# Kernel tuning notes

Hardware: AMD Instinct MI355X
Metric: run time of the kernel (lower is better)

## Reference

```python
import jax, jax.numpy as jnp
import numpy as np

B, T, I, H = 32768, 200, 6, 6
FF, OUT = 128, 12


def setup_inputs() -> dict:
    key = jax.random.key(0)
    ks = jax.random.split(key, 10)
    s = lambda fan_in: 1.0 / np.sqrt(fan_in)
    inp = {
        "x": jax.random.normal(ks[0], (B, T, I), dtype=jnp.float32),
        # PyTorch LSTM params (gate order i, f, g, o)
        "W_ih": jax.random.uniform(ks[1], (4 * H, I), jnp.float32, -s(H), s(H)),
        "W_hh": jax.random.uniform(ks[2], (4 * H, H), jnp.float32, -s(H), s(H)),
        "b_ih": jax.random.uniform(ks[3], (4 * H,), jnp.float32, -s(H), s(H)),
        "b_hh": jax.random.uniform(ks[4], (4 * H,), jnp.float32, -s(H), s(H)),
        # MLP head (Dropout is identity in eval mode)
        "W1": jax.random.uniform(ks[5], (FF, T * H), jnp.float32, -s(T * H), s(T * H)),
        "b1": jax.random.uniform(ks[6], (FF,), jnp.float32, -s(T * H), s(T * H)),
        "W2": jax.random.uniform(ks[7], (OUT, FF), jnp.float32, -s(FF), s(FF)),
        "b2": jax.random.uniform(ks[8], (OUT,), jnp.float32, -s(FF), s(FF)),
    }
    return inp


def _lstm(x, W_ih, W_hh, b_ih, b_hh):
    # x: [B, T, I] -> hidden sequence [B, T, H]
    # Precompute input projections for all timesteps at once: [T, B, 4H]
    xg = jnp.einsum("bti,gi->tbg", x, W_ih) + (b_ih + b_hh)
    h0 = jnp.zeros((x.shape[0], H), x.dtype)
    c0 = jnp.zeros((x.shape[0], H), x.dtype)

    def step(carry, xg_t):
        h, c = carry
        gates = xg_t + h @ W_hh.T  # [B, 4H]
        i, f, g, o = jnp.split(gates, 4, axis=-1)
        i = jax.nn.sigmoid(i)
        f = jax.nn.sigmoid(f)
        g = jnp.tanh(g)
        o = jax.nn.sigmoid(o)
        c = f * c + i * g
        h = o * jnp.tanh(c)
        return (h, c), h

    _, hs = jax.lax.scan(step, (h0, c0), xg)  # hs: [T, B, H]
    return jnp.transpose(hs, (1, 0, 2))  # [B, T, H]


def reference(x, W_ih, W_hh, b_ih, b_hh, W1, b1, W2, b2):
    hs = _lstm(x, W_ih, W_hh, b_ih, b_hh)          # [B, T, H]
    flat = hs.reshape(hs.shape[0], -1)             # [B, T*H]
    hid = jax.nn.relu(flat @ W1.T + b1)            # [B, 128]
    return hid @ W2.T + b2                         # [B, 12]
```

## Files before the change

kernel.cpp:

```cpp
#include <hip/hip_runtime.h>
#include <hip/hip_bf16.h>

#define Bn   32768
#define Tn   200
#define In   6
#define Hn   6
#define FFn  128
#define OUTn 12
#define KP   1600

typedef __attribute__((ext_vector_type(2))) float          f32x2;
typedef __attribute__((ext_vector_type(4))) float          f32x4;
typedef __attribute__((ext_vector_type(8))) short          bf16x8;
typedef __attribute__((ext_vector_type(4))) unsigned short u16x4;
typedef __attribute__((ext_vector_type(8))) unsigned short u16x8;

#define LOG2E 1.442695041f

__device__ __forceinline__ f32x2 pkfma(f32x2 a, f32x2 b, f32x2 c) {
#if __has_builtin(__builtin_elementwise_fma)
    return __builtin_elementwise_fma(a, b, c);
#else
    return a * b + c;
#endif
}
__device__ __forceinline__ float swap1(float v) {
    return __int_as_float(__builtin_amdgcn_mov_dpp(__float_as_int(v), 0xB1, 0xF, 0xF, true));
}
__device__ __forceinline__ unsigned short f2bf(float v) {
    unsigned u = __float_as_uint(v);
    unsigned r = u + 0x7FFFu + ((u >> 16) & 1u);
    return (unsigned short)(r >> 16);
}

#define BAR() do {                                          \
    asm volatile("s_waitcnt lgkmcnt(0)" ::: "memory");      \
    __builtin_amdgcn_sched_barrier(0);                      \
    __builtin_amdgcn_s_barrier();                           \
    __builtin_amdgcn_sched_barrier(0);                      \
} while (0)

__global__ void prep_kernel(const float* __restrict__ W1, unsigned short* __restrict__ W1p) {
    int idx = blockIdx.x * 256 + threadIdx.x;
    if (idx >= FFn * KP) return;
    int ff = idx / KP, kp = idx - ff * KP;
    int t = kp >> 3, p = kp & 7;
    float v = 0.f;
    if (p != 3 && p != 7) {
        int h = (p < 3) ? p : (p - 1);
        v = W1[ff * (Tn * Hn) + t * Hn + h];
    }
    W1p[idx] = f2bf(v);
}

__global__ __launch_bounds__(256, 1)
void fused_kernel(const float* __restrict__ x,
                  const float* __restrict__ W_ih, const float* __restrict__ W_hh,
                  const float* __restrict__ b_ih, const float* __restrict__ b_hh,
                  const unsigned short* __restrict__ W1p,
                  const float* __restrict__ b1,
                  const float* __restrict__ W2, const float* __restrict__ b2,
                  float* __restrict__ out)
{
    __shared__ unsigned short htile[2][8][128][8];
    __shared__ unsigned short hidS[128][136];
    __shared__ float          W2s[OUTn * FFn];

    const int tid  = threadIdx.x;
    const int sloc = tid >> 1;
    const int role = tid & 1;
    const int b0   = blockIdx.x * 128;
    const int wv   = tid >> 6;
    const int l    = tid & 63;
    const int lr   = l & 15;
    const int lg   = l >> 4;

    f32x2 Wx[6][6], Wh[6][6], bias2[6];
    #pragma unroll
    for (int gt = 0; gt < 4; ++gt) {
        #pragma unroll
        for (int m = 0; m < 3; ++m) {
            const int j = gt * 3 + m;
            const int p = j >> 1, hf = j & 1;
            const int row = gt * 6 + role * 3 + m;
            const float sc = (gt == 2) ? (2.f * LOG2E) : (-LOG2E);
            #pragma unroll
            for (int k = 0; k < 6; ++k) Wx[p][k][hf] = sc * W_ih[row * 6 + k];
            #pragma unroll
            for (int k = 0; k < 3; ++k) Wh[p][k][hf]     = sc * W_hh[row * 6 + role * 3 + k];
            #pragma unroll
            for (int k = 0; k < 3; ++k) Wh[p][3 + k][hf] = sc * W_hh[row * 6 + (1 - role) * 3 + k];
            bias2[p][hf] = sc * (b_ih[row] + b_hh[row]);
        }
    }

    float hOwn[3] = {0.f, 0.f, 0.f}, hOth[3] = {0.f, 0.f, 0.f}, cS[3] = {0.f, 0.f, 0.f};

    f32x4 acc[8][2];
    #pragma unroll
    for (int m = 0; m < 8; ++m)
        #pragma unroll
        for (int n = 0; n < 2; ++n)
            acc[m][n] = (f32x4){0.f, 0.f, 0.f, 0.f};

    const f32x4* xb4 = (const f32x4*)(x + (size_t)(b0 + sloc) * (Tn * In));

    const unsigned short* wrow[2];
    #pragma unroll
    for (int n = 0; n < 2; ++n) wrow[n] = W1p + (size_t)(wv * 32 + n * 16 + lr) * KP;

    auto LOADB = [&](int g, bf16x8 (&bf)[2][2]) {
        #pragma unroll
        for (int kc = 0; kc < 2; ++kc)
            #pragma unroll
            for (int n = 0; n < 2; ++n)
                bf[kc][n] = *((const bf16x8*)&wrow[n][g * 64 + kc * 32 + lg * 8]);
    };

    auto STEPS4 = [&](const f32x4 (&bx)[6], int slot, int sbase) {
        #pragma unroll
        for (int s = 0; s < 4; ++s) {
            float xv[6];
            #pragma unroll
            for (int k = 0; k < 6; ++k) { const int fl = s * 6 + k; xv[k] = bx[fl >> 2][fl & 3]; }
            f32x2 a2[6];
            #pragma unroll
            for (int p = 0; p < 6; ++p) a2[p] = bias2[p];
            #pragma unroll
            for (int k = 0; k < 6; ++k) {
                const f32x2 xs = (f32x2){xv[k], xv[k]};
                #pragma unroll
                for (int p = 0; p < 6; ++p) a2[p] = pkfma(Wx[p][k], xs, a2[p]);
            }
            #pragma unroll
            for (int k = 0; k < 3; ++k) {
                const f32x2 hs = (f32x2){hOwn[k], hOwn[k]};
                #pragma unroll
                for (int p = 0; p < 6; ++p) a2[p] = pkfma(Wh[p][k], hs, a2[p]);
            }
            #pragma unroll
            for (int k = 0; k < 3; ++k) {
                const f32x2 hs = (f32x2){hOth[k], hOth[k]};
                #pragma unroll
                for (int p = 0; p < 6; ++p) a2[p] = pkfma(Wh[p][3 + k], hs, a2[p]);
            }
            float av[12];
            #pragma unroll
            for (int p = 0; p < 6; ++p) { av[2 * p] = a2[p][0]; av[2 * p + 1] = a2[p][1]; }

            unsigned short hb[3];
            #pragma unroll
            for (int m = 0; m < 3; ++m) {
                const float Ei = __builtin_amdgcn_exp2f(av[m]);
                const float Ef = __builtin_amdgcn_exp2f(av[3 + m]);
                const float Eg = __builtin_amdgcn_exp2f(av[6 + m]);
                const float Eo = __builtin_amdgcn_exp2f(av[9 + m]);
                const float fv = __builtin_amdgcn_rcpf(1.f + Ef);
                const float ig = (Eg - 1.f) *
                                 __builtin_amdgcn_rcpf((1.f + Ei) * (1.f + Eg));
                float c = fmaf(fv, cS[m], ig);
                c = fminf(fmaxf(c, -30.f), 30.f);
                cS[m] = c;
                const float Ec = __builtin_amdgcn_exp2f(2.f * LOG2E * c);
                const float hv = (Ec - 1.f) *
                                 __builtin_amdgcn_rcpf((1.f + Eo) * (1.f + Ec));
                hOwn[m] = hv;
                hOth[m] = swap1(hv);
                hb[m]   = f2bf(hv);
            }
            u16x4 hw; hw.x = hb[0]; hw.y = hb[1]; hw.z = hb[2]; hw.w = 0;
            *((u16x4*)&htile[slot][sbase + s][sloc][role * 4]) = hw;
        }
    };

    auto MFMAG8 = [&](int slot, const bf16x8 (&bf)[2][2]) {
        #pragma unroll
        for (int kc = 0; kc < 2; ++kc) {
            bf16x8 af[8];
            #pragma unroll
            for (int m = 0; m < 8; ++m)
                af[m] = *((const bf16x8*)&htile[slot][kc * 4 + lg][m * 16 + lr][0]);
            #pragma unroll
            for (int n = 0; n < 2; ++n)
                #pragma unroll
                for (int m = 0; m < 8; ++m)
                    acc[m][n] = __builtin_amdgcn_mfma_f32_16x16x32_bf16(af[m], bf[kc][n], acc[m][n], 0, 0, 0);
        }
    };

    f32x4 bufA[6], bufB[6];
    #pragma unroll
    for (int q = 0; q < 6; ++q) bufA[q] = xb4[q];
    bf16x8 bfg[2][2];

    for (int g = 0; g < 25; ++g) {
        #pragma unroll
        for (int q = 0; q < 6; ++q) bufB[q] = xb4[(2 * g + 1) * 6 + q];
        STEPS4(bufA, g & 1, 0);
        LOADB(g, bfg);
        if (g < 24) {
            #pragma unroll
            for (int q = 0; q < 6; ++q) bufA[q] = xb4[(2 * g + 2) * 6 + q];
        }
        STEPS4(bufB, g & 1, 4);
        BAR();
        MFMAG8(g & 1, bfg);
    }

    float b1v[2];
    #pragma unroll
    for (int n = 0; n < 2; ++n) b1v[n] = b1[wv * 32 + n * 16 + lr];
    #pragma unroll
    for (int m = 0; m < 8; ++m)
        #pragma unroll
        for (int n = 0; n < 2; ++n)
            #pragma unroll
            for (int r = 0; r < 4; ++r)
                hidS[m * 16 + lg * 4 + r][wv * 32 + n * 16 + lr] =
                    f2bf(fmaxf(acc[m][n][r] + b1v[n], 0.f));
    for (int q = tid; q < OUTn * FFn; q += 256) W2s[q] = W2[q];
    __syncthreads();

    const int s2 = tid >> 1;
    const int half = tid & 1;
    float oa[6];
    #pragma unroll
    for (int jj = 0; jj < 6; ++jj) oa[jj] = b2[half * 6 + jj];
    for (int k8 = 0; k8 < 16; ++k8) {
        const u16x8 hv8 = *((const u16x8*)&hidS[s2][k8 * 8]);
        #pragma unroll
        for (int e = 0; e < 8; ++e) {
            const float hv = __uint_as_float(((unsigned)(unsigned short)hv8[e]) << 16);
            const int k = k8 * 8 + e;
            #pragma unroll
            for (int jj = 0; jj < 6; ++jj)
                oa[jj] = fmaf(hv, W2s[(half * 6 + jj) * FFn + k], oa[jj]);
        }
    }
    float* op = out + (size_t)(b0 + s2) * OUTn + half * 6;
    #pragma unroll
    for (int jj = 0; jj < 6; ++jj) op[jj] = oa[jj];
}

extern "C" void kernel_launch(void* const* d_in, const int* in_sizes, int n_in,
                              void* d_out, int out_size, void* d_ws, size_t ws_size,
                              hipStream_t stream) {
    const float* x    = (const float*)d_in[0];
    const float* W_ih = (const float*)d_in[1];
    const float* W_hh = (const float*)d_in[2];
    const float* b_ih = (const float*)d_in[3];
    const float* b_hh = (const float*)d_in[4];
    const float* W1   = (const float*)d_in[5];
    const float* b1   = (const float*)d_in[6];
    const float* W2   = (const float*)d_in[7];
    const float* b2   = (const float*)d_in[8];
    unsigned short* W1p = (unsigned short*)d_ws;
    float* out = (float*)d_out;

    prep_kernel<<<(FFn * KP + 255) / 256, 256, 0, stream>>>(W1, W1p);
    fused_kernel<<<Bn / 128, 256, 0, stream>>>(x, W_ih, W_hh, b_ih, b_hh,
                                               W1p, b1, W2, b2, out);
}
```

Measured before the change: 123.8 us.

## Warp-specialize fused kernel into LSTM producer and MFMA consumer waves

Splits each 512-thread block into four producer waves that run the LSTM recurrence and write fp32 hidden states to a double-buffered LDS tile, and four consumer waves that convert those states to bf16 with packed converts and run the W1 MFMA accumulation. The goal is to take MFMA and W1 loads off the latency-bound recurrence path so the two overlap. The cell-state clamp becomes a clamp on the exponent argument only, and the W2 head is split over four lanes per sample. In exchange the fp32 tile doubles LDS traffic for the hidden states, and the barrier counts between producer and consumer loops must match exactly.

```diff
diff --git a/kernel.cpp b/kernel.cpp
--- a/kernel.cpp
+++ b/kernel.cpp
@@ -12,8 +12,8 @@
 typedef __attribute__((ext_vector_type(2))) float          f32x2;
 typedef __attribute__((ext_vector_type(4))) float          f32x4;
 typedef __attribute__((ext_vector_type(8))) short          bf16x8;
-typedef __attribute__((ext_vector_type(4))) unsigned short u16x4;
 typedef __attribute__((ext_vector_type(8))) unsigned short u16x8;
+typedef __attribute__((ext_vector_type(4))) unsigned int   u32x4;
 
 #define LOG2E 1.442695041f
 
@@ -31,6 +31,11 @@
     unsigned u = __float_as_uint(v);
     unsigned r = u + 0x7FFFu + ((u >> 16) & 1u);
     return (unsigned short)(r >> 16);
+}
+__device__ __forceinline__ unsigned cvt_pk_bf16(float a, float b) {
+    unsigned r;
+    asm("v_cvt_pk_bf16_f32 %0, %1, %2" : "=v"(r) : "v"(a), "v"(b));
+    return r;
 }
 
 #define BAR() do {                                          \
@@ -53,7 +58,7 @@
     W1p[idx] = f2bf(v);
 }
 
-__global__ __launch_bounds__(256, 1)
+__global__ __launch_bounds__(512, 2)
 void fused_kernel(const float* __restrict__ x,
                   const float* __restrict__ W_ih, const float* __restrict__ W_hh,
                   const float* __restrict__ b_ih, const float* __restrict__ b_hh,
@@ -62,170 +67,195 @@
                   const float* __restrict__ W2, const float* __restrict__ b2,
                   float* __restrict__ out)
 {
-    __shared__ unsigned short htile[2][8][128][8];
+    __shared__ float          htile32[2][8][128][8];
     __shared__ unsigned short hidS[128][136];
     __shared__ float          W2s[OUTn * FFn];
 
-    const int tid  = threadIdx.x;
-    const int sloc = tid >> 1;
-    const int role = tid & 1;
-    const int b0   = blockIdx.x * 128;
-    const int wv   = tid >> 6;
-    const int l    = tid & 63;
-    const int lr   = l & 15;
-    const int lg   = l >> 4;
-
-    f32x2 Wx[6][6], Wh[6][6], bias2[6];
+    const int tid = threadIdx.x;
+    const int wv  = tid >> 6;
+    const int b0  = blockIdx.x * 128;
+
+    if (wv < 4) {
+        const int sloc = tid >> 1;
+        const int role = tid & 1;
+
+        f32x2 Wx[6][6], Wh[6][6], bias2[6];
+        #pragma unroll
+        for (int gt = 0; gt < 4; ++gt) {
+            #pragma unroll
+            for (int m = 0; m < 3; ++m) {
+                const int j = gt * 3 + m;
+                const int p = j >> 1, hf = j & 1;
+                const int row = gt * 6 + role * 3 + m;
+                const float sc = (gt == 2) ? (2.f * LOG2E) : (-LOG2E);
+                #pragma unroll
+                for (int k = 0; k < 6; ++k) Wx[p][k][hf] = sc * W_ih[row * 6 + k];
+                #pragma unroll
+                for (int k = 0; k < 3; ++k) Wh[p][k][hf]     = sc * W_hh[row * 6 + role * 3 + k];
+                #pragma unroll
+                for (int k = 0; k < 3; ++k) Wh[p][3 + k][hf] = sc * W_hh[row * 6 + (1 - role) * 3 + k];
+                bias2[p][hf] = sc * (b_ih[row] + b_hh[row]);
+            }
+        }
+
+        float hOwn[3] = {0.f, 0.f, 0.f}, hOth[3] = {0.f, 0.f, 0.f}, cS[3] = {0.f, 0.f, 0.f};
+
+        const f32x4* xb4 = (const f32x4*)(x + (size_t)(b0 + sloc) * (Tn * In));
+
+        auto STEPS4 = [&](const f32x4 (&bx)[6], int slot, int sbase) {
+            #pragma unroll
+            for (int s = 0; s < 4; ++s) {
+                float xv[6];
+                #pragma unroll
+                for (int k = 0; k < 6; ++k) { const int fl = s * 6 + k; xv[k] = bx[fl >> 2][fl & 3]; }
+                f32x2 a2[6];
+                #pragma unroll
+                for (int p = 0; p < 6; ++p) a2[p] = bias2[p];
+                #pragma unroll
+                for (int k = 0; k < 6; ++k) {
+                    const f32x2 xs = (f32x2){xv[k], xv[k]};
+                    #pragma unroll
+                    for (int p = 0; p < 6; ++p) a2[p] = pkfma(Wx[p][k], xs, a2[p]);
+                }
+                #pragma unroll
+                for (int k = 0; k < 3; ++k) {
+                    const f32x2 hs = (f32x2){hOwn[k], hOwn[k]};
+                    #pragma unroll
+                    for (int p = 0; p < 6; ++p) a2[p] = pkfma(Wh[p][k], hs, a2[p]);
+                }
+                #pragma unroll
+                for (int k = 0; k < 3; ++k) {
+                    const f32x2 hs = (f32x2){hOth[k], hOth[k]};
+                    #pragma unroll
+                    for (int p = 0; p < 6; ++p) a2[p] = pkfma(Wh[p][3 + k], hs, a2[p]);
+                }
+                float av[12];
+                #pragma unroll
+                for (int p = 0; p < 6; ++p) { av[2 * p] = a2[p][0]; av[2 * p + 1] = a2[p][1]; }
+
+                float hq[3];
+                #pragma unroll
+                for (int m = 0; m < 3; ++m) {
+                    const float Ei = __builtin_amdgcn_exp2f(av[m]);
+                    const float Ef = __builtin_amdgcn_exp2f(av[3 + m]);
+                    const float Eg = __builtin_amdgcn_exp2f(av[6 + m]);
+                    const float Eo = __builtin_amdgcn_exp2f(av[9 + m]);
+                    const float fv = __builtin_amdgcn_rcpf(1.f + Ef);
+                    const float ig = (Eg - 1.f) *
+                                     __builtin_amdgcn_rcpf((1.f + Ei) * (1.f + Eg));
+                    const float c  = fmaf(fv, cS[m], ig);
+                    cS[m] = c;
+                    const float Ec = __builtin_amdgcn_exp2f(fminf(2.f * LOG2E * c, 60.f));
+                    const float hv = (Ec - 1.f) *
+                                     __builtin_amdgcn_rcpf((1.f + Eo) * (1.f + Ec));
+                    hOwn[m] = hv;
+                    hOth[m] = swap1(hv);
+                    hq[m]   = hv;
+                }
+                const f32x4 hw4 = (f32x4){hq[0], hq[1], hq[2], 0.f};
+                *((f32x4*)&htile32[slot][sbase + s][sloc][role * 4]) = hw4;
+            }
+        };
+
+        f32x4 bufA[6], bufB[6];
+        #pragma unroll
+        for (int q = 0; q < 6; ++q) bufA[q] = xb4[q];
+
+        for (int g = 0; g < 25; ++g) {
+            #pragma unroll
+            for (int q = 0; q < 6; ++q) bufB[q] = xb4[(2 * g + 1) * 6 + q];
+            STEPS4(bufA, g & 1, 0);
+            if (g < 24) {
+                #pragma unroll
+                for (int q = 0; q < 6; ++q) bufA[q] = xb4[(2 * g + 2) * 6 + q];
+            }
+            STEPS4(bufB, g & 1, 4);
+            BAR();
+        }
+        for (int q = tid; q < OUTn * FFn; q += 256) W2s[q] = W2[q];
+
+    } else {
+        const int wv2 = wv - 4;
+        const int l   = tid & 63;
+        const int lr  = l & 15;
+        const int lg  = l >> 4;
+
+        const unsigned short* wrow[2];
+        #pragma unroll
+        for (int n = 0; n < 2; ++n) wrow[n] = W1p + (size_t)(wv2 * 32 + n * 16 + lr) * KP;
+
+        f32x4 acc[8][2];
+        #pragma unroll
+        for (int m = 0; m < 8; ++m)
+            #pragma unroll
+            for (int n = 0; n < 2; ++n)
+                acc[m][n] = (f32x4){0.f, 0.f, 0.f, 0.f};
+
+        auto LOADB = [&](int g, bf16x8 (&bf)[2][2]) {
+            #pragma unroll
+            for (int kc = 0; kc < 2; ++kc)
+                #pragma unroll
+                for (int n = 0; n < 2; ++n)
+                    bf[kc][n] = *((const bf16x8*)&wrow[n][g * 64 + kc * 32 + lg * 8]);
+        };
+
+        auto MFMAG8 = [&](int slot, const bf16x8 (&bf)[2][2]) {
+            #pragma unroll
+            for (int kc = 0; kc < 2; ++kc) {
+                bf16x8 af[8];
+                #pragma unroll
+                for (int m = 0; m < 8; ++m) {
+                    const f32x4 lo = *((const f32x4*)&htile32[slot][kc * 4 + lg][m * 16 + lr][0]);
+                    const f32x4 hi = *((const f32x4*)&htile32[slot][kc * 4 + lg][m * 16 + lr][4]);
+                    u32x4 w;
+                    w[0] = cvt_pk_bf16(lo[0], lo[1]);
+                    w[1] = cvt_pk_bf16(lo[2], lo[3]);
+                    w[2] = cvt_pk_bf16(hi[0], hi[1]);
+                    w[3] = cvt_pk_bf16(hi[2], hi[3]);
+                    af[m] = *((const bf16x8*)&w);
+                }
+                #pragma unroll
+                for (int n = 0; n < 2; ++n)
+                    #pragma unroll
+                    for (int m = 0; m < 8; ++m)
+                        acc[m][n] = __builtin_amdgcn_mfma_f32_16x16x32_bf16(af[m], bf[kc][n], acc[m][n], 0, 0, 0);
+            }
+        };
+
+        bf16x8 bfA[2][2], bfB[2][2];
+        LOADB(0, bfA);
+        for (int gg = 0; gg < 12; ++gg) {
+            BAR();
+            LOADB(2 * gg + 1, bfB);
+            MFMAG8(0, bfA);
+            BAR();
+            const int gn = (2 * gg + 2 < 25) ? (2 * gg + 2) : 24;
+            LOADB(gn, bfA);
+            MFMAG8(1, bfB);
+        }
+        BAR();
+        MFMAG8(0, bfA);
+
+        float b1v[2];
+        #pragma unroll
+        for (int n = 0; n < 2; ++n) b1v[n] = b1[wv2 * 32 + n * 16 + lr];
+        #pragma unroll
+        for (int m = 0; m < 8; ++m)
+            #pragma unroll
+            for (int n = 0; n < 2; ++n)
+                #pragma unroll
+                for (int r = 0; r < 4; ++r)
+                    hidS[m * 16 + lg * 4 + r][wv2 * 32 + n * 16 + lr] =
+                        f2bf(fmaxf(acc[m][n][r] + b1v[n], 0.f));
+    }
+
+    __syncthreads();
+
+    const int s2 = tid >> 2;
+    const int q  = tid & 3;
+    float oa[3];
     #pragma unroll
-    for (int gt = 0; gt < 4; ++gt) {
-        #pragma unroll
-        for (int m = 0; m < 3; ++m) {
-            const int j = gt * 3 + m;
-            const int p = j >> 1, hf = j & 1;
-            const int row = gt * 6 + role * 3 + m;
-            const float sc = (gt == 2) ? (2.f * LOG2E) : (-LOG2E);
-            #pragma unroll
-            for (int k = 0; k < 6; ++k) Wx[p][k][hf] = sc * W_ih[row * 6 + k];
-            #pragma unroll
-            for (int k = 0; k < 3; ++k) Wh[p][k][hf]     = sc * W_hh[row * 6 + role * 3 + k];
-            #pragma unroll
-            for (int k = 0; k < 3; ++k) Wh[p][3 + k][hf] = sc * W_hh[row * 6 + (1 - role) * 3 + k];
-            bias2[p][hf] = sc * (b_ih[row] + b_hh[row]);
-        }
-    }
-
-    float hOwn[3] = {0.f, 0.f, 0.f}, hOth[3] = {0.f, 0.f, 0.f}, cS[3] = {0.f, 0.f, 0.f};
-
-    f32x4 acc[8][2];
-    #pragma unroll
-    for (int m = 0; m < 8; ++m)
-        #pragma unroll
-        for (int n = 0; n < 2; ++n)
-            acc[m][n] = (f32x4){0.f, 0.f, 0.f, 0.f};
-
-    const f32x4* xb4 = (const f32x4*)(x + (size_t)(b0 + sloc) * (Tn * In));
-
-    const unsigned short* wrow[2];
-    #pragma unroll
-    for (int n = 0; n < 2; ++n) wrow[n] = W1p + (size_t)(wv * 32 + n * 16 + lr) * KP;
-
-    auto LOADB = [&](int g, bf16x8 (&bf)[2][2]) {
-        #pragma unroll
-        for (int kc = 0; kc < 2; ++kc)
-            #pragma unroll
-            for (int n = 0; n < 2; ++n)
-                bf[kc][n] = *((const bf16x8*)&wrow[n][g * 64 + kc * 32 + lg * 8]);
-    };
-
-    auto STEPS4 = [&](const f32x4 (&bx)[6], int slot, int sbase) {
-        #pragma unroll
-        for (int s = 0; s < 4; ++s) {
-            float xv[6];
-            #pragma unroll
-            for (int k = 0; k < 6; ++k) { const int fl = s * 6 + k; xv[k] = bx[fl >> 2][fl & 3]; }
-            f32x2 a2[6];
-            #pragma unroll
-            for (int p = 0; p < 6; ++p) a2[p] = bias2[p];
-            #pragma unroll
-            for (int k = 0; k < 6; ++k) {
-                const f32x2 xs = (f32x2){xv[k], xv[k]};
-                #pragma unroll
-                for (int p = 0; p < 6; ++p) a2[p] = pkfma(Wx[p][k], xs, a2[p]);
-            }
-            #pragma unroll
-            for (int k = 0; k < 3; ++k) {
-                const f32x2 hs = (f32x2){hOwn[k], hOwn[k]};
-                #pragma unroll
-                for (int p = 0; p < 6; ++p) a2[p] = pkfma(Wh[p][k], hs, a2[p]);
-            }
-            #pragma unroll
-            for (int k = 0; k < 3; ++k) {
-                const f32x2 hs = (f32x2){hOth[k], hOth[k]};
-                #pragma unroll
-                for (int p = 0; p < 6; ++p) a2[p] = pkfma(Wh[p][3 + k], hs, a2[p]);
-            }
-            float av[12];
-            #pragma unroll
-            for (int p = 0; p < 6; ++p) { av[2 * p] = a2[p][0]; av[2 * p + 1] = a2[p][1]; }
-
-            unsigned short hb[3];
-            #pragma unroll
-            for (int m = 0; m < 3; ++m) {
-                const float Ei = __builtin_amdgcn_exp2f(av[m]);
-                const float Ef = __builtin_amdgcn_exp2f(av[3 + m]);
-                const float Eg = __builtin_amdgcn_exp2f(av[6 + m]);
-                const float Eo = __builtin_amdgcn_exp2f(av[9 + m]);
-                const float fv = __builtin_amdgcn_rcpf(1.f + Ef);
-                const float ig = (Eg - 1.f) *
-                                 __builtin_amdgcn_rcpf((1.f + Ei) * (1.f + Eg));
-                float c = fmaf(fv, cS[m], ig);
-                c = fminf(fmaxf(c, -30.f), 30.f);
-                cS[m] = c;
-                const float Ec = __builtin_amdgcn_exp2f(2.f * LOG2E * c);
-                const float hv = (Ec - 1.f) *
-                                 __builtin_amdgcn_rcpf((1.f + Eo) * (1.f + Ec));
-                hOwn[m] = hv;
-                hOth[m] = swap1(hv);
-                hb[m]   = f2bf(hv);
-            }
-            u16x4 hw; hw.x = hb[0]; hw.y = hb[1]; hw.z = hb[2]; hw.w = 0;
-            *((u16x4*)&htile[slot][sbase + s][sloc][role * 4]) = hw;
-        }
-    };
-
-    auto MFMAG8 = [&](int slot, const bf16x8 (&bf)[2][2]) {
-        #pragma unroll
-        for (int kc = 0; kc < 2; ++kc) {
-            bf16x8 af[8];
-            #pragma unroll
-            for (int m = 0; m < 8; ++m)
-                af[m] = *((const bf16x8*)&htile[slot][kc * 4 + lg][m * 16 + lr][0]);
-            #pragma unroll
-            for (int n = 0; n < 2; ++n)
-                #pragma unroll
-                for (int m = 0; m < 8; ++m)
-                    acc[m][n] = __builtin_amdgcn_mfma_f32_16x16x32_bf16(af[m], bf[kc][n], acc[m][n], 0, 0, 0);
-        }
-    };
-
-    f32x4 bufA[6], bufB[6];
-    #pragma unroll
-    for (int q = 0; q < 6; ++q) bufA[q] = xb4[q];
-    bf16x8 bfg[2][2];
-
-    for (int g = 0; g < 25; ++g) {
-        #pragma unroll
-        for (int q = 0; q < 6; ++q) bufB[q] = xb4[(2 * g + 1) * 6 + q];
-        STEPS4(bufA, g & 1, 0);
-        LOADB(g, bfg);
-        if (g < 24) {
-            #pragma unroll
-            for (int q = 0; q < 6; ++q) bufA[q] = xb4[(2 * g + 2) * 6 + q];
-        }
-        STEPS4(bufB, g & 1, 4);
-        BAR();
-        MFMAG8(g & 1, bfg);
-    }
-
-    float b1v[2];
-    #pragma unroll
-    for (int n = 0; n < 2; ++n) b1v[n] = b1[wv * 32 + n * 16 + lr];
-    #pragma unroll
-    for (int m = 0; m < 8; ++m)
-        #pragma unroll
-        for (int n = 0; n < 2; ++n)
-            #pragma unroll
-            for (int r = 0; r < 4; ++r)
-                hidS[m * 16 + lg * 4 + r][wv * 32 + n * 16 + lr] =
-                    f2bf(fmaxf(acc[m][n][r] + b1v[n], 0.f));
-    for (int q = tid; q < OUTn * FFn; q += 256) W2s[q] = W2[q];
-    __syncthreads();
-
-    const int s2 = tid >> 1;
-    const int half = tid & 1;
-    float oa[6];
-    #pragma unroll
-    for (int jj = 0; jj < 6; ++jj) oa[jj] = b2[half * 6 + jj];
+    for (int jj = 0; jj < 3; ++jj) oa[jj] = b2[q * 3 + jj];
     for (int k8 = 0; k8 < 16; ++k8) {
         const u16x8 hv8 = *((const u16x8*)&hidS[s2][k8 * 8]);
         #pragma unroll
@@ -233,13 +263,13 @@
             const float hv = __uint_as_float(((unsigned)(unsigned short)hv8[e]) << 16);
             const int k = k8 * 8 + e;
             #pragma unroll
-            for (int jj = 0; jj < 6; ++jj)
-                oa[jj] = fmaf(hv, W2s[(half * 6 + jj) * FFn + k], oa[jj]);
+            for (int jj = 0; jj < 3; ++jj)
+                oa[jj] = fmaf(hv, W2s[(q * 3 + jj) * FFn + k], oa[jj]);
         }
     }
-    float* op = out + (size_t)(b0 + s2) * OUTn + half * 6;
+    float* op = out + (size_t)(b0 + s2) * OUTn + q * 3;
     #pragma unroll
-    for (int jj = 0; jj < 6; ++jj) op[jj] = oa[jj];
+    for (int jj = 0; jj < 3; ++jj) op[jj] = oa[jj];
 }
 
 extern "C" void kernel_launch(void* const* d_in, const int* in_sizes, int n_in,
@@ -258,6 +288,6 @@
     float* out = (float*)d_out;
 
     prep_kernel<<<(FFn * KP + 255) / 256, 256, 0, stream>>>(W1, W1p);
-    fused_kernel<<<Bn / 128, 256, 0, stream>>>(x, W_ih, W_hh, b_ih, b_hh,
+    fused_kernel<<<Bn / 128, 512, 0, stream>>>(x, W_ih, W_hh, b_ih, b_hh,
                                                W1p, b1, W2, b2, out);
 }
```

Result: slower. 126.5 us (+2.2%).
